# Performance work log

Hardware: AMD Instinct MI355X
Metric: run time of the kernel (lower is better)

Reference implementation:

```python
import jax, jax.numpy as jnp
import numpy as np

K = 5  # kernel_size per dim (dim=2 -> 25 kernels), B-spline degree 1, open spline


def spline_conv(x, edge_index, pseudo, W, root, bias):
    # x: [N, Cin], pseudo: [E, 2] in [0,1], W: [K*K, Cin, Cout]
    N = x.shape[0]
    src, dst = edge_index[0], edge_index[1]
    # Transform node features with every kernel weight once: [N, K*K, Cout]
    xk = jnp.einsum('ni,kio->nko', x, W)
    # Degree-1 open B-spline basis: v = u*(K-1); frac/1-frac weights over 2 knots per dim
    v = pseudo * (K - 1)
    bot = jnp.floor(v)
    frac = v - bot
    bot = bot.astype(jnp.int32)
    msg = jnp.zeros((src.shape[0], W.shape[2]), dtype=x.dtype)
    for s0 in (0, 1):
        for s1 in (0, 1):
            b0 = frac[:, 0] if s0 else (1.0 - frac[:, 0])
            b1 = frac[:, 1] if s1 else (1.0 - frac[:, 1])
            basis = b0 * b1  # [E]
            idx = (jnp.clip(bot[:, 0] + s0, 0, K - 1)
                   + K * jnp.clip(bot[:, 1] + s1, 0, K - 1))  # [E]
            msg = msg + basis[:, None] * xk[src, idx]  # gather [E, Cout]
    # scatter-max aggregation into target nodes; empty nodes -> 0 (PyG convention)
    agg = jax.ops.segment_max(msg, dst, num_segments=N)
    agg = jnp.where(jnp.isfinite(agg), agg, jnp.zeros_like(agg))
    return agg + x @ root + bias


def setup_inputs() -> dict:
    key = jax.random.key(0)
    ks = jax.random.split(key, 8)
    N, E, C = 50000, 1600000, 64
    Cin = C
    s = 1.0 / np.sqrt(25 * Cin)
    return {
        'x': jax.random.normal(ks[0], (N, C), dtype=jnp.float32),
        'edge_index': jax.random.randint(ks[1], (2, E), 0, N, dtype=jnp.int32),
        'edge_attr': jax.random.uniform(ks[2], (E, 2), dtype=jnp.float32),
        'W1': jax.random.normal(ks[3], (25, C, C), dtype=jnp.float32) * s,
        'root1': jax.random.normal(ks[4], (C, C), dtype=jnp.float32) / np.sqrt(C),
        'bias1': jnp.zeros((C,), dtype=jnp.float32),
        'W2': jax.random.normal(ks[5], (25, C, C), dtype=jnp.float32) * s,
        'root2': jax.random.normal(ks[6], (C, C), dtype=jnp.float32) / np.sqrt(C),
        'bias2': jnp.zeros((C,), dtype=jnp.float32),
    }


def reference(x, edge_index, edge_attr, W1, root1, bias1, W2, root2, bias2):
    h = jax.nn.relu(spline_conv(x, edge_index, edge_attr, W1, root1, bias1))
    out = spline_conv(h, edge_index, edge_attr, W2, root2, bias2)
    return out
```

## Files before the change

kernel.cpp:

```cpp
#include <hip/hip_runtime.h>
#include <hip/hip_bf16.h>
#include <math.h>

#define CHANNELS 64
#define KK 25
#define NBLK 26
#define NCOL (NBLK * CHANNELS)
#define NTILES (NCOL / 16)
#define ROWP 2560
#define GROUP_TILES 8
#define GROUP_BYTES (GROUP_TILES * 2048)
#define NGROUPS (NTILES / GROUP_TILES)
#define G_SPLIT 6

typedef __attribute__((ext_vector_type(8))) short bf16x8;
typedef __attribute__((ext_vector_type(4))) float f32x4;
typedef __attribute__((ext_vector_type(2))) float f32x2;
typedef unsigned int u32;

__device__ __forceinline__ u32 f2bfu(float f) {
    u32 u = __float_as_uint(f);
    return (u + 0x7FFFu + ((u >> 16) & 1u)) >> 16;
}
__device__ __forceinline__ short f2bf(float f) { return (short)f2bfu(f); }

__device__ __forceinline__ void async_copy16(const void* g, void* l) {
    __builtin_amdgcn_global_load_lds(
        (const __attribute__((address_space(1))) u32*)g,
        (__attribute__((address_space(3))) u32*)l, 16, 0, 0);
}


__global__ __launch_bounds__(256) void scan_a(const u32* __restrict__ counts,
                                              u32* __restrict__ bsum, int N) {
    const int t = threadIdx.x;
    const int base = blockIdx.x * 1024 + t * 4;
    uint4 v = make_uint4(0, 0, 0, 0);
    if (base + 3 < N) v = *(const uint4*)(counts + base);
    else {
        if (base < N)     v.x = counts[base];
        if (base + 1 < N) v.y = counts[base + 1];
        if (base + 2 < N) v.z = counts[base + 2];
    }
    u32 s = v.x + v.y + v.z + v.w;
    for (int off = 32; off; off >>= 1) s += __shfl_down(s, off, 64);
    __shared__ u32 red[4];
    if ((t & 63) == 0) red[t >> 6] = s;
    __syncthreads();
    if (t == 0) bsum[blockIdx.x] = red[0] + red[1] + red[2] + red[3];
}

__global__ __launch_bounds__(64) void scan_b(u32* __restrict__ bsum, int nb) {
    const int lane = threadIdx.x;
    u32 run = 0;
    for (int base = 0; base < nb; base += 64) {
        u32 v = (base + lane < nb) ? bsum[base + lane] : 0u;
        const u32 orig = v;
        for (int off = 1; off < 64; off <<= 1) {
            u32 u = __shfl_up(v, off, 64);
            if (lane >= off) v += u;
        }
        if (base + lane < nb) bsum[base + lane] = run + v - orig;
        run += __shfl(v, 63, 64);
    }
}

__global__ __launch_bounds__(256) void scan_c(const u32* __restrict__ counts,
                                              const u32* __restrict__ bsum,
                                              u32* __restrict__ cursor, int N) {
    const int t = threadIdx.x;
    const int base = blockIdx.x * 1024 + t * 4;
    uint4 v = make_uint4(0, 0, 0, 0);
    if (base + 3 < N) v = *(const uint4*)(counts + base);
    else {
        if (base < N)     v.x = counts[base];
        if (base + 1 < N) v.y = counts[base + 1];
        if (base + 2 < N) v.z = counts[base + 2];
    }
    __shared__ u32 ps[256];
    ps[t] = v.x + v.y + v.z + v.w;
    __syncthreads();
    for (int off = 1; off < 256; off <<= 1) {
        u32 u = (t >= off) ? ps[t - off] : 0u;
        __syncthreads();
        ps[t] += u;
        __syncthreads();
    }
    u32 ex = ((t > 0) ? ps[t - 1] : 0u) + bsum[blockIdx.x];
    if (base < N)     cursor[base]     = ex;
    if (base + 1 < N) cursor[base + 1] = ex + v.x;
    if (base + 2 < N) cursor[base + 2] = ex + v.x + v.y;
    if (base + 3 < N) cursor[base + 3] = ex + v.x + v.y + v.z;
    if (base <= N - 1 && N - 1 <= base + 3)
        cursor[N] = ex + v.x + v.y + v.z + v.w;
}


__global__ __launch_bounds__(256) void prep_w(const float* __restrict__ W,
                                              const float* __restrict__ root,
                                              __hip_bfloat16* __restrict__ Wb) {
    int idx = blockIdx.x * 256 + threadIdx.x;
    if (idx >= NTILES * 2 * 64 * 8) return;
    int j = idx & 7;
    int l = (idx >> 3) & 63;
    int q = (idx >> 9) & 1;
    int t = idx >> 10;
    int cell = t >> 2;
    int o    = 4 * (l & 15) + (t & 3);
    int k    = q * 32 + (l >> 4) * 8 + j;
    float src = (cell < KK) ? W[cell * 4096 + k * 64 + o] : root[k * 64 + o];
    ((unsigned short*)Wb)[idx] = (unsigned short)f2bf(src);
}

__device__ __forceinline__ void gemm_body(
    const float* __restrict__ X, const __hip_bfloat16* __restrict__ Wb,
    char* __restrict__ XK, float* __restrict__ rootf, int N, int gr0, int gr1)
{
    __shared__ __align__(16) char lds[2][GROUP_BYTES];
    const int lane = threadIdx.x & 63;
    const int wv   = threadIdx.x >> 6;
    const int rb   = blockIdx.x * 64 + wv * 16;
    const int m    = lane & 15;
    const int quad = lane >> 4;

    const int rowc = min(rb + m, N - 1);
    const float* __restrict__ xp = X + (size_t)rowc * CHANNELS + quad * 8;
    float af[16];
    *(float4*)(af)      = *(const float4*)(xp);
    *(float4*)(af + 4)  = *(const float4*)(xp + 4);
    *(float4*)(af + 8)  = *(const float4*)(xp + 32);
    *(float4*)(af + 12) = *(const float4*)(xp + 36);
    bf16x8 A0, A1;
#pragma unroll
    for (int j = 0; j < 8; ++j) { A0[j] = f2bf(af[j]); A1[j] = f2bf(af[8 + j]); }

    const int r0 = rb + quad * 4;
    const int rmax = N - r0;
    char* __restrict__ orow0 = XK + (size_t)r0 * ROWP;

    const char* __restrict__ wbc = (const char*)Wb;
#define STAGE(g, buf)                                                          \
    {                                                                          \
        const char* gsrc = wbc + (size_t)(g) * GROUP_BYTES + wv * 4096 + lane * 16; \
        char* lbase = lds[buf] + wv * 4096;                                    \
        async_copy16(gsrc,        lbase);                                      \
        async_copy16(gsrc + 1024, lbase + 1024);                               \
        async_copy16(gsrc + 2048, lbase + 2048);                               \
        async_copy16(gsrc + 3072, lbase + 3072);                               \
    }

    STAGE(gr0, 0)
    for (int g = gr0; g < gr1; ++g) {
        const int li = (g - gr0) & 1;
        __syncthreads();
        if (g + 1 < gr1) STAGE(g + 1, li ^ 1)
        const char* lb = lds[li] + lane * 16;
#pragma unroll
        for (int cc = 0; cc < 2; ++cc) {
            const char* cb = lb + cc * 8192;
            f32x4 acc0 = {0.f, 0.f, 0.f, 0.f};
            f32x4 acc1 = {0.f, 0.f, 0.f, 0.f};
            f32x4 acc2 = {0.f, 0.f, 0.f, 0.f};
            f32x4 acc3 = {0.f, 0.f, 0.f, 0.f};
            acc0 = __builtin_amdgcn_mfma_f32_16x16x32_bf16(A0, *(const bf16x8*)(cb),        acc0, 0, 0, 0);
            acc0 = __builtin_amdgcn_mfma_f32_16x16x32_bf16(A1, *(const bf16x8*)(cb + 1024), acc0, 0, 0, 0);
            acc1 = __builtin_amdgcn_mfma_f32_16x16x32_bf16(A0, *(const bf16x8*)(cb + 2048), acc1, 0, 0, 0);
            acc1 = __builtin_amdgcn_mfma_f32_16x16x32_bf16(A1, *(const bf16x8*)(cb + 3072), acc1, 0, 0, 0);
            acc2 = __builtin_amdgcn_mfma_f32_16x16x32_bf16(A0, *(const bf16x8*)(cb + 4096), acc2, 0, 0, 0);
            acc2 = __builtin_amdgcn_mfma_f32_16x16x32_bf16(A1, *(const bf16x8*)(cb + 5120), acc2, 0, 0, 0);
            acc3 = __builtin_amdgcn_mfma_f32_16x16x32_bf16(A0, *(const bf16x8*)(cb + 6144), acc3, 0, 0, 0);
            acc3 = __builtin_amdgcn_mfma_f32_16x16x32_bf16(A1, *(const bf16x8*)(cb + 7168), acc3, 0, 0, 0);
            const int kc = g * 2 + cc;
            if (kc < KK) {
                const int d1 = kc / 5;
                const int d0 = kc - 5 * d1;
                const int boff = d1 * 512 + d0 * 128 + 4 * m;
#pragma unroll
                for (int i = 0; i < 4; ++i) {
                    if (i < rmax) {
                        u32 p = __builtin_amdgcn_cvt_pk_fp8_f32(acc0[i], acc1[i], 0u, false);
                        p = __builtin_amdgcn_cvt_pk_fp8_f32(acc2[i], acc3[i], p, true);
                        char* orow = orow0 + (size_t)i * ROWP;
                        if (d0 <= 3) *(u32*)(orow + boff) = p;
                        if (d0 >= 1) *(u32*)(orow + boff - 64) = p;
                    }
                }
            } else {
#pragma unroll
                for (int i = 0; i < 4; ++i) {
                    if (i < rmax) {
                        *(float4*)(rootf + (size_t)(r0 + i) * CHANNELS + 4 * m) =
                            make_float4(acc0[i], acc1[i], acc2[i], acc3[i]);
                    }
                }
            }
        }
    }
#undef STAGE
}

__global__ __launch_bounds__(256) void gemm_hist(
    const float* __restrict__ X, const __hip_bfloat16* __restrict__ Wb,
    char* __restrict__ XK, float* __restrict__ rootf, int N, int gemm_blocks,
    const int* __restrict__ ei, u32* __restrict__ counts,
    u32* __restrict__ rank, int E)
{
    if ((int)blockIdx.x >= gemm_blocks) {
        int e = ((int)blockIdx.x - gemm_blocks) * 256 + threadIdx.x;
        if (e < E) rank[e] = atomicAdd(&counts[ei[E + e]], 1u);
        return;
    }
    gemm_body(X, Wb, XK, rootf, N, 0, G_SPLIT);
}

__global__ __launch_bounds__(256) void gemm_scatter(
    const float* __restrict__ X, const __hip_bfloat16* __restrict__ Wb,
    char* __restrict__ XK, float* __restrict__ rootf, int N, int gemm_blocks,
    const int* __restrict__ ei, const float* __restrict__ ps,
    const u32* __restrict__ rank, const u32* __restrict__ cursor,
    uint2* __restrict__ sorted, int E, int gr0, int gr1)
{
    if ((int)blockIdx.x >= gemm_blocks) {
        int e = ((int)blockIdx.x - gemm_blocks) * 256 + threadIdx.x;
        if (e >= E) return;
        const int src = ei[e];
        const int dst = ei[E + e];
        const float v0 = ps[2 * e]     * 4.0f;
        const float v1 = ps[2 * e + 1] * 4.0f;
        const int p0 = max(min((int)floorf(v0), 3), 0);
        const int p1 = max(min((int)floorf(v1), 3), 0);
        const float f0 = v0 - (float)p0;
        const float f1 = v1 - (float)p1;
        const u32 f0q = min((u32)(f0 * 65536.0f), 65535u);
        const u32 f1q = min((u32)(f1 * 65536.0f), 65535u);
        uint2 rec;
        rec.x = (u32)src | ((u32)p0 << 16) | ((u32)p1 << 19);
        rec.y = f0q | (f1q << 16);
        sorted[cursor[dst] + rank[e]] = rec;
        return;
    }
    gemm_body(X, Wb, XK, rootf, N, gr0, gr1);
}

__global__ __launch_bounds__(256) void agg_node_p(
    const uint2* __restrict__ sorted, const u32* __restrict__ cursor,
    const char* __restrict__ XK, const float* __restrict__ rootf,
    const float* __restrict__ bias, float* __restrict__ out, int N, int relu,
    int node_blocks, const float* __restrict__ Wsrc,
    const float* __restrict__ rootsrc, __hip_bfloat16* __restrict__ Wbdst)
{
    if ((int)blockIdx.x >= node_blocks) {
        int idx = ((int)blockIdx.x - node_blocks) * 256 + threadIdx.x;
        if (idx < NTILES * 2 * 64 * 8) {
            int j = idx & 7;
            int l = (idx >> 3) & 63;
            int q = (idx >> 9) & 1;
            int t = idx >> 10;
            int cell = t >> 2;
            int o    = 4 * (l & 15) + (t & 3);
            int k    = q * 32 + (l >> 4) * 8 + j;
            float s = (cell < KK) ? Wsrc[cell * 4096 + k * 64 + o] : rootsrc[k * 64 + o];
            ((unsigned short*)Wbdst)[idx] = (unsigned short)f2bf(s);
        }
        return;
    }
    const int lane = threadIdx.x & 63;
    const int n = blockIdx.x * 4 + (threadIdx.x >> 6);
    if (n >= N) return;
    const int q = lane >> 4, j = lane & 15;
    const int beg = (int)cursor[n];
    const int end = (int)cursor[n + 1];

    float m0 = -INFINITY, m1 = -INFINITY, m2 = -INFINITY, m3 = -INFINITY;
    if (beg < end) {
        const int last = end - 1;
#define GATHP(r, gll, ghl, glh, ghh)                                           \
        {                                                                      \
            const char* b_ = XK + (size_t)((r).x & 0xffff) * ROWP + (j << 2);  \
            const int o_ = (((int)((r).x >> 16) & 7)                           \
                            + (((int)((r).x >> 19) & 7) << 2)) << 7;           \
            gll = *(const u32*)(b_ + o_);                                      \
            ghl = *(const u32*)(b_ + o_ + 64);                                 \
            glh = *(const u32*)(b_ + o_ + 512);                                \
            ghh = *(const u32*)(b_ + o_ + 576);                                \
        }
        uint2 rA = sorted[min(beg + q,      last)];
        uint2 rB = sorted[min(beg + 4 + q,  last)];
        uint2 rC = sorted[min(beg + 8 + q,  last)];
        u32 a0, a1, a2, a3, b0, b1, b2, b3, c0, c1, c2, c3;
        GATHP(rA, a0, a1, a2, a3)
        GATHP(rB, b0, b1, b2, b3)
        for (int i = beg; i < end; i += 4) {
            uint2 rD = sorted[min(i + 12 + q, last)];
            GATHP(rC, c0, c1, c2, c3)
            const float f0 = (float)(rA.y & 0xffff) * (1.0f / 65536.0f);
            const float f1 = (float)(rA.y >> 16)    * (1.0f / 65536.0f);
            const float w00 = (1.f - f0) * (1.f - f1);
            const float w10 = f0 * (1.f - f1);
            const float w01 = (1.f - f0) * f1;
            const float w11 = f0 * f1;
            f32x2 s01 = __builtin_amdgcn_cvt_pk_f32_fp8(a0, false) * w00
                      + __builtin_amdgcn_cvt_pk_f32_fp8(a1, false) * w10
                      + __builtin_amdgcn_cvt_pk_f32_fp8(a2, false) * w01
                      + __builtin_amdgcn_cvt_pk_f32_fp8(a3, false) * w11;
            f32x2 s23 = __builtin_amdgcn_cvt_pk_f32_fp8(a0, true)  * w00
                      + __builtin_amdgcn_cvt_pk_f32_fp8(a1, true)  * w10
                      + __builtin_amdgcn_cvt_pk_f32_fp8(a2, true)  * w01
                      + __builtin_amdgcn_cvt_pk_f32_fp8(a3, true)  * w11;
            m0 = fmaxf(m0, s01.x); m1 = fmaxf(m1, s01.y);
            m2 = fmaxf(m2, s23.x); m3 = fmaxf(m3, s23.y);
            rA = rB; rB = rC; rC = rD;
            a0 = b0; a1 = b1; a2 = b2; a3 = b3;
            b0 = c0; b1 = c1; b2 = c2; b3 = c3;
        }
#undef GATHP
    }
    m0 = fmaxf(m0, __shfl_xor(m0, 16, 64)); m0 = fmaxf(m0, __shfl_xor(m0, 32, 64));
    m1 = fmaxf(m1, __shfl_xor(m1, 16, 64)); m1 = fmaxf(m1, __shfl_xor(m1, 32, 64));
    m2 = fmaxf(m2, __shfl_xor(m2, 16, 64)); m2 = fmaxf(m2, __shfl_xor(m2, 32, 64));
    m3 = fmaxf(m3, __shfl_xor(m3, 16, 64)); m3 = fmaxf(m3, __shfl_xor(m3, 32, 64));
    const float a0 = isfinite(m0) ? m0 : 0.f;
    const float a1 = isfinite(m1) ? m1 : 0.f;
    const float a2 = isfinite(m2) ? m2 : 0.f;
    const float a3 = isfinite(m3) ? m3 : 0.f;

    const float4 rv = *(const float4*)(rootf + (size_t)n * CHANNELS + 4 * j);
    const float4 bv = *(const float4*)(bias + 4 * j);
    float r0 = a0 + rv.x + bv.x;
    float r1 = a1 + rv.y + bv.y;
    float r2 = a2 + rv.z + bv.z;
    float r3 = a3 + rv.w + bv.w;
    if (relu) {
        r0 = fmaxf(r0, 0.f); r1 = fmaxf(r1, 0.f);
        r2 = fmaxf(r2, 0.f); r3 = fmaxf(r3, 0.f);
    }
    if (q == 0)
        *(float4*)(out + (size_t)n * CHANNELS + 4 * j) = make_float4(r0, r1, r2, r3);
}

extern "C" void kernel_launch(void* const* d_in, const int* in_sizes, int n_in,
                              void* d_out, int out_size, void* d_ws, size_t ws_size,
                              hipStream_t stream) {
    const float* x     = (const float*)d_in[0];
    const int*   ei    = (const int*)d_in[1];
    const float* ps    = (const float*)d_in[2];
    const float* W1    = (const float*)d_in[3];
    const float* root1 = (const float*)d_in[4];
    const float* bias1 = (const float*)d_in[5];
    const float* W2    = (const float*)d_in[6];
    const float* root2 = (const float*)d_in[7];
    const float* bias2 = (const float*)d_in[8];
    float* out = (float*)d_out;

    const int N = in_sizes[0] / CHANNELS;
    const int E = in_sizes[1] / 2;

    char* ws = (char*)d_ws;
    char* xk = ws;
    size_t off = (size_t)N * ROWP;
    float* h = (float*)(ws + off);
    off += (size_t)N * CHANNELS * sizeof(float);
    float* rootf = (float*)(ws + off);
    off += (size_t)N * CHANNELS * sizeof(float);
    uint2* sorted = (uint2*)(ws + off);
    off += (size_t)E * sizeof(uint2);
    u32* rank = (u32*)(ws + off);
    off += (size_t)E * sizeof(u32);
    u32* counts = (u32*)(ws + off);
    off += (size_t)N * 4;
    __hip_bfloat16* Wb = (__hip_bfloat16*)(ws + off);
    off += (size_t)NTILES * 2 * 64 * 8 * 2;
    u32* cursor = (u32*)(ws + off);
    off += ((size_t)N + 1) * 4;
    u32* bsum = (u32*)(ws + off);

    const int prep_blocks = (NTILES * 2 * 64 * 8 + 255) / 256;
    const int gemm_blocks = (N + 63) / 64;
    const int node_blocks = (N + 3) / 4;
    const int edgeT_blocks = (E + 255) / 256;
    const int scan_blocks = (N + 1023) / 1024;

    hipMemsetAsync(counts, 0, (size_t)N * 4, stream);
    prep_w<<<prep_blocks, 256, 0, stream>>>(W1, root1, Wb);

    gemm_hist<<<gemm_blocks + edgeT_blocks, 256, 0, stream>>>(
        x, Wb, xk, rootf, N, gemm_blocks, ei, counts, rank, E);

    scan_a<<<scan_blocks, 256, 0, stream>>>(counts, bsum, N);
    scan_b<<<1, 64, 0, stream>>>(bsum, scan_blocks);
    scan_c<<<scan_blocks, 256, 0, stream>>>(counts, bsum, cursor, N);

    gemm_scatter<<<gemm_blocks + edgeT_blocks, 256, 0, stream>>>(
        x, Wb, xk, rootf, N, gemm_blocks, ei, ps, rank, cursor, sorted, E, G_SPLIT, NGROUPS);
    agg_node_p<<<node_blocks + prep_blocks, 256, 0, stream>>>(
        sorted, cursor, xk, rootf, bias1, h, N, 1, node_blocks, W2, root2, Wb);

    gemm_scatter<<<gemm_blocks, 256, 0, stream>>>(
        h, Wb, xk, rootf, N, gemm_blocks, ei, ps, rank, cursor, sorted, 0, 0, NGROUPS);
    agg_node_p<<<node_blocks, 256, 0, stream>>>(
        sorted, cursor, xk, rootf, bias2, out, N, 0, node_blocks, W2, root2, Wb);
}
```

Baseline: 397.9 us.

## Run full first-layer GEMM with histogram, split scatter into standalone vectorized kernel

New measurement: 421.3 us. 1.06x slower.

```diff
diff --git a/kernel.cpp b/kernel.cpp
--- a/kernel.cpp
+++ b/kernel.cpp
@@ -11,7 +11,6 @@
 #define GROUP_TILES 8
 #define GROUP_BYTES (GROUP_TILES * 2048)
 #define NGROUPS (NTILES / GROUP_TILES)
-#define G_SPLIT 6
 
 typedef __attribute__((ext_vector_type(8))) short bf16x8;
 typedef __attribute__((ext_vector_type(4))) float f32x4;
@@ -206,40 +205,73 @@
     u32* __restrict__ rank, int E)
 {
     if ((int)blockIdx.x >= gemm_blocks) {
-        int e = ((int)blockIdx.x - gemm_blocks) * 256 + threadIdx.x;
-        if (e < E) rank[e] = atomicAdd(&counts[ei[E + e]], 1u);
+        const int e0 = ((int)blockIdx.x - gemm_blocks) * 1024 + threadIdx.x * 4;
+        if (e0 + 3 < E) {
+            const int4 d = *(const int4*)(ei + E + e0);
+            const u32 r0 = atomicAdd(&counts[d.x], 1u);
+            const u32 r1 = atomicAdd(&counts[d.y], 1u);
+            const u32 r2 = atomicAdd(&counts[d.z], 1u);
+            const u32 r3 = atomicAdd(&counts[d.w], 1u);
+            *(uint4*)(rank + e0) = make_uint4(r0, r1, r2, r3);
+        } else {
+            for (int k = 0; k < 4; ++k)
+                if (e0 + k < E)
+                    rank[e0 + k] = atomicAdd(&counts[ei[E + e0 + k]], 1u);
+        }
         return;
     }
-    gemm_body(X, Wb, XK, rootf, N, 0, G_SPLIT);
-}
-
-__global__ __launch_bounds__(256) void gemm_scatter(
+    gemm_body(X, Wb, XK, rootf, N, 0, NGROUPS);
+}
+
+__global__ __launch_bounds__(256) void gemm_only(
     const float* __restrict__ X, const __hip_bfloat16* __restrict__ Wb,
-    char* __restrict__ XK, float* __restrict__ rootf, int N, int gemm_blocks,
+    char* __restrict__ XK, float* __restrict__ rootf, int N)
+{
+    gemm_body(X, Wb, XK, rootf, N, 0, NGROUPS);
+}
+
+__device__ __forceinline__ uint2 mkrec(int src, float v0f, float v1f) {
+    const float v0 = v0f * 4.0f, v1 = v1f * 4.0f;
+    const int p0 = max(min((int)floorf(v0), 3), 0);
+    const int p1 = max(min((int)floorf(v1), 3), 0);
+    const float f0 = v0 - (float)p0;
+    const float f1 = v1 - (float)p1;
+    const u32 f0q = min((u32)(f0 * 65536.0f), 65535u);
+    const u32 f1q = min((u32)(f1 * 65536.0f), 65535u);
+    uint2 rec;
+    rec.x = (u32)src | ((u32)p0 << 16) | ((u32)p1 << 19);
+    rec.y = f0q | (f1q << 16);
+    return rec;
+}
+
+__global__ __launch_bounds__(256) void edge_scatter(
     const int* __restrict__ ei, const float* __restrict__ ps,
     const u32* __restrict__ rank, const u32* __restrict__ cursor,
-    uint2* __restrict__ sorted, int E, int gr0, int gr1)
+    uint2* __restrict__ sorted, int E)
 {
-    if ((int)blockIdx.x >= gemm_blocks) {
-        int e = ((int)blockIdx.x - gemm_blocks) * 256 + threadIdx.x;
-        if (e >= E) return;
-        const int src = ei[e];
-        const int dst = ei[E + e];
-        const float v0 = ps[2 * e]     * 4.0f;
-        const float v1 = ps[2 * e + 1] * 4.0f;
-        const int p0 = max(min((int)floorf(v0), 3), 0);
-        const int p1 = max(min((int)floorf(v1), 3), 0);
-        const float f0 = v0 - (float)p0;
-        const float f1 = v1 - (float)p1;
-        const u32 f0q = min((u32)(f0 * 65536.0f), 65535u);
-        const u32 f1q = min((u32)(f1 * 65536.0f), 65535u);
-        uint2 rec;
-        rec.x = (u32)src | ((u32)p0 << 16) | ((u32)p1 << 19);
-        rec.y = f0q | (f1q << 16);
-        sorted[cursor[dst] + rank[e]] = rec;
-        return;
-    }
-    gemm_body(X, Wb, XK, rootf, N, gr0, gr1);
+    const int e0 = blockIdx.x * 1024 + threadIdx.x * 4;
+    if (e0 + 3 < E) {
+        const int4 s  = *(const int4*)(ei + e0);
+        const int4 d  = *(const int4*)(ei + E + e0);
+        const float4 pa = *(const float4*)(ps + 2 * e0);
+        const float4 pb = *(const float4*)(ps + 2 * e0 + 4);
+        const uint4 rk = *(const uint4*)(rank + e0);
+        const u32 c0 = cursor[d.x];
+        const u32 c1 = cursor[d.y];
+        const u32 c2 = cursor[d.z];
+        const u32 c3 = cursor[d.w];
+        sorted[c0 + rk.x] = mkrec(s.x, pa.x, pa.y);
+        sorted[c1 + rk.y] = mkrec(s.y, pa.z, pa.w);
+        sorted[c2 + rk.z] = mkrec(s.z, pb.x, pb.y);
+        sorted[c3 + rk.w] = mkrec(s.w, pb.z, pb.w);
+    } else {
+        for (int k = 0; k < 4; ++k) {
+            const int e = e0 + k;
+            if (e < E)
+                sorted[cursor[ei[E + e]] + rank[e]] =
+                    mkrec(ei[e], ps[2 * e], ps[2 * e + 1]);
+        }
+    }
 }
 
 __global__ __launch_bounds__(256) void agg_node_p(
@@ -377,26 +409,25 @@
     const int prep_blocks = (NTILES * 2 * 64 * 8 + 255) / 256;
     const int gemm_blocks = (N + 63) / 64;
     const int node_blocks = (N + 3) / 4;
-    const int edgeT_blocks = (E + 255) / 256;
+    const int edgeQ_blocks = (E + 1023) / 1024;
     const int scan_blocks = (N + 1023) / 1024;
 
     hipMemsetAsync(counts, 0, (size_t)N * 4, stream);
     prep_w<<<prep_blocks, 256, 0, stream>>>(W1, root1, Wb);
 
-    gemm_hist<<<gemm_blocks + edgeT_blocks, 256, 0, stream>>>(
+    gemm_hist<<<gemm_blocks + edgeQ_blocks, 256, 0, stream>>>(
         x, Wb, xk, rootf, N, gemm_blocks, ei, counts, rank, E);
 
     scan_a<<<scan_blocks, 256, 0, stream>>>(counts, bsum, N);
     scan_b<<<1, 64, 0, stream>>>(bsum, scan_blocks);
     scan_c<<<scan_blocks, 256, 0, stream>>>(counts, bsum, cursor, N);
 
-    gemm_scatter<<<gemm_blocks + edgeT_blocks, 256, 0, stream>>>(
-        x, Wb, xk, rootf, N, gemm_blocks, ei, ps, rank, cursor, sorted, E, G_SPLIT, NGROUPS);
+    edge_scatter<<<edgeQ_blocks, 256, 0, stream>>>(ei, ps, rank, cursor, sorted, E);
+
     agg_node_p<<<node_blocks + prep_blocks, 256, 0, stream>>>(
         sorted, cursor, xk, rootf, bias1, h, N, 1, node_blocks, W2, root2, Wb);
 
-    gemm_scatter<<<gemm_blocks, 256, 0, stream>>>(
-        h, Wb, xk, rootf, N, gemm_blocks, ei, ps, rank, cursor, sorted, 0, 0, NGROUPS);
+    gemm_only<<<gemm_blocks, 256, 0, stream>>>(h, Wb, xk, rootf, N);
     agg_node_p<<<node_blocks, 256, 0, stream>>>(
         sorted, cursor, xk, rootf, bias2, out, N, 0, node_blocks, W2, root2, Wb);
 }
```

## Warp-specialize GEMM blocks with extra waves doing edge histogram and scatter

Applied to the files above, without the earlier changes.

New measurement: 461.4 us. 16.0% more time.

```diff
diff --git a/kernel.cpp b/kernel.cpp
--- a/kernel.cpp
+++ b/kernel.cpp
@@ -199,47 +199,79 @@
 #undef STAGE
 }
 
-__global__ __launch_bounds__(256) void gemm_hist(
+__global__ __launch_bounds__(512) void gemm_hist(
     const float* __restrict__ X, const __hip_bfloat16* __restrict__ Wb,
-    char* __restrict__ XK, float* __restrict__ rootf, int N, int gemm_blocks,
+    char* __restrict__ XK, float* __restrict__ rootf, int N,
     const int* __restrict__ ei, u32* __restrict__ counts,
     u32* __restrict__ rank, int E)
 {
-    if ((int)blockIdx.x >= gemm_blocks) {
-        int e = ((int)blockIdx.x - gemm_blocks) * 256 + threadIdx.x;
-        if (e < E) rank[e] = atomicAdd(&counts[ei[E + e]], 1u);
-        return;
-    }
-    gemm_body(X, Wb, XK, rootf, N, 0, G_SPLIT);
-}
-
-__global__ __launch_bounds__(256) void gemm_scatter(
+    if (threadIdx.x < 256) {
+        gemm_body(X, Wb, XK, rootf, N, 0, G_SPLIT);
+    } else {
+        const int tid = blockIdx.x * 256 + (threadIdx.x - 256);
+        const int ET  = (int)gridDim.x * 256;
+        const int rounds = (E + ET - 1) / ET;
+        int r = 0;
+        for (int ch = 0; ch < G_SPLIT; ++ch) {
+            const int rend = ((ch + 1) * rounds) / G_SPLIT;
+            for (; r < rend; ++r) {
+                const int e = tid + r * ET;
+                if (e < E) rank[e] = atomicAdd(&counts[ei[E + e]], 1u);
+            }
+            __syncthreads();
+        }
+    }
+}
+
+__device__ __forceinline__ uint2 mkrec(int src, float v0f, float v1f) {
+    const float v0 = v0f * 4.0f, v1 = v1f * 4.0f;
+    const int p0 = max(min((int)floorf(v0), 3), 0);
+    const int p1 = max(min((int)floorf(v1), 3), 0);
+    const float f0 = v0 - (float)p0;
+    const float f1 = v1 - (float)p1;
+    const u32 f0q = min((u32)(f0 * 65536.0f), 65535u);
+    const u32 f1q = min((u32)(f1 * 65536.0f), 65535u);
+    uint2 rec;
+    rec.x = (u32)src | ((u32)p0 << 16) | ((u32)p1 << 19);
+    rec.y = f0q | (f1q << 16);
+    return rec;
+}
+
+__global__ __launch_bounds__(512) void gemm_scatter(
     const float* __restrict__ X, const __hip_bfloat16* __restrict__ Wb,
-    char* __restrict__ XK, float* __restrict__ rootf, int N, int gemm_blocks,
+    char* __restrict__ XK, float* __restrict__ rootf, int N,
     const int* __restrict__ ei, const float* __restrict__ ps,
     const u32* __restrict__ rank, const u32* __restrict__ cursor,
-    uint2* __restrict__ sorted, int E, int gr0, int gr1)
+    uint2* __restrict__ sorted, int E)
 {
-    if ((int)blockIdx.x >= gemm_blocks) {
-        int e = ((int)blockIdx.x - gemm_blocks) * 256 + threadIdx.x;
-        if (e >= E) return;
-        const int src = ei[e];
-        const int dst = ei[E + e];
-        const float v0 = ps[2 * e]     * 4.0f;
-        const float v1 = ps[2 * e + 1] * 4.0f;
-        const int p0 = max(min((int)floorf(v0), 3), 0);
-        const int p1 = max(min((int)floorf(v1), 3), 0);
-        const float f0 = v0 - (float)p0;
-        const float f1 = v1 - (float)p1;
-        const u32 f0q = min((u32)(f0 * 65536.0f), 65535u);
-        const u32 f1q = min((u32)(f1 * 65536.0f), 65535u);
-        uint2 rec;
-        rec.x = (u32)src | ((u32)p0 << 16) | ((u32)p1 << 19);
-        rec.y = f0q | (f1q << 16);
-        sorted[cursor[dst] + rank[e]] = rec;
-        return;
-    }
-    gemm_body(X, Wb, XK, rootf, N, gr0, gr1);
+    constexpr int NCH = NGROUPS - G_SPLIT;
+    if (threadIdx.x < 256) {
+        gemm_body(X, Wb, XK, rootf, N, G_SPLIT, NGROUPS);
+    } else {
+        const int tid = blockIdx.x * 256 + (threadIdx.x - 256);
+        const int ET  = (int)gridDim.x * 256;
+        const int rounds = (E + ET - 1) / ET;
+        int r = 0;
+        for (int ch = 0; ch < NCH; ++ch) {
+            const int rend = ((ch + 1) * rounds) / NCH;
+            for (; r < rend; ++r) {
+                const int e = tid + r * ET;
+                if (e < E) {
+                    const int dst = ei[E + e];
+                    sorted[cursor[dst] + rank[e]] =
+                        mkrec(ei[e], ps[2 * e], ps[2 * e + 1]);
+                }
+            }
+            __syncthreads();
+        }
+    }
+}
+
+__global__ __launch_bounds__(256) void gemm_only(
+    const float* __restrict__ X, const __hip_bfloat16* __restrict__ Wb,
+    char* __restrict__ XK, float* __restrict__ rootf, int N)
+{
+    gemm_body(X, Wb, XK, rootf, N, 0, NGROUPS);
 }
 
 __global__ __launch_bounds__(256) void agg_node_p(
@@ -377,26 +409,25 @@
     const int prep_blocks = (NTILES * 2 * 64 * 8 + 255) / 256;
     const int gemm_blocks = (N + 63) / 64;
     const int node_blocks = (N + 3) / 4;
-    const int edgeT_blocks = (E + 255) / 256;
     const int scan_blocks = (N + 1023) / 1024;
 
     hipMemsetAsync(counts, 0, (size_t)N * 4, stream);
     prep_w<<<prep_blocks, 256, 0, stream>>>(W1, root1, Wb);
 
-    gemm_hist<<<gemm_blocks + edgeT_blocks, 256, 0, stream>>>(
-        x, Wb, xk, rootf, N, gemm_blocks, ei, counts, rank, E);
+    gemm_hist<<<gemm_blocks, 512, 0, stream>>>(
+        x, Wb, xk, rootf, N, ei, counts, rank, E);
 
     scan_a<<<scan_blocks, 256, 0, stream>>>(counts, bsum, N);
     scan_b<<<1, 64, 0, stream>>>(bsum, scan_blocks);
     scan_c<<<scan_blocks, 256, 0, stream>>>(counts, bsum, cursor, N);
 
-    gemm_scatter<<<gemm_blocks + edgeT_blocks, 256, 0, stream>>>(
-        x, Wb, xk, rootf, N, gemm_blocks, ei, ps, rank, cursor, sorted, E, G_SPLIT, NGROUPS);
+    gemm_scatter<<<gemm_blocks, 512, 0, stream>>>(
+        x, Wb, xk, rootf, N, ei, ps, rank, cursor, sorted, E);
+
     agg_node_p<<<node_blocks + prep_blocks, 256, 0, stream>>>(
         sorted, cursor, xk, rootf, bias1, h, N, 1, node_blocks, W2, root2, Wb);
 
-    gemm_scatter<<<gemm_blocks, 256, 0, stream>>>(
-        h, Wb, xk, rootf, N, gemm_blocks, ei, ps, rank, cursor, sorted, 0, 0, NGROUPS);
+    gemm_only<<<gemm_blocks, 256, 0, stream>>>(h, Wb, xk, rootf, N);
     agg_node_p<<<node_blocks, 256, 0, stream>>>(
         sorted, cursor, xk, rootf, bias2, out, N, 0, node_blocks, W2, root2, Wb);
 }
```
